# Performance work log

Measured on AMD Instinct MI355X. Metric: run time of the kernel, lower is better.

## Reference

```python
import jax, jax.numpy as jnp
import numpy as np

K = 1024
D = 256
BETA = 0.25


def setup_inputs() -> dict:
    key = jax.random.key(0)
    k1, k2 = jax.random.split(key)
    inputs = jax.random.normal(k1, (16, D, 4096), dtype=jnp.float32)  # (B, D, T)
    # embedding.weight.data.uniform_(-1/K, 1/K)
    weight = jax.random.uniform(k2, (K, D), dtype=jnp.float32, minval=-1.0 / K, maxval=1.0 / K)
    return {"inputs": inputs, "weight": weight}


def reference(inputs, weight):
    B, Dd, T = inputs.shape
    x = jnp.transpose(inputs, (0, 2, 1))          # (B, T, D)
    flat = x.reshape(-1, Dd)                      # (N, D), N = B*T
    in_sqr = jnp.sum(flat * flat, axis=1, keepdims=True)     # (N, 1)
    embed_sqr = jnp.sum(weight * weight, axis=1)             # (K,)
    dis = in_sqr + embed_sqr - 2.0 * (flat @ weight.T)       # (N, K)
    ind = jnp.argmin(dis, axis=1)                            # (N,)
    quant = weight[ind].reshape(B, T, Dd)                    # gather == one-hot @ weight
    vq = jnp.mean((jax.lax.stop_gradient(quant) - x) ** 2)
    commit = jnp.mean((quant - jax.lax.stop_gradient(x)) ** 2)
    vq_loss = BETA * vq + commit
    quant_st = x + jax.lax.stop_gradient(quant - x)          # straight-through
    N = flat.shape[0]
    counts = jnp.zeros((K,), dtype=jnp.float32).at[ind].add(1.0)
    avg_probs = counts / N
    perp = jnp.exp(-jnp.sum(avg_probs * jnp.log(avg_probs + 1e-10)))
    return jnp.transpose(quant_st, (0, 2, 1)), vq_loss, perp
```

## Files before the change

### kernel.cpp

```cpp
#include <hip/hip_runtime.h>
#include <hip/hip_bf16.h>


#define DD   256
#define KK   1024
#define TT   4096
#define BBB  16
#define NROW (BBB*TT)

typedef _Float16 half8 __attribute__((ext_vector_type(8)));
typedef float f32x4 __attribute__((ext_vector_type(4)));

__device__ __forceinline__ unsigned umaxu(unsigned a, unsigned b) { return a > b ? a : b; }
__device__ __forceinline__ unsigned uminu(unsigned a, unsigned b) { return a < b ? a : b; }

__device__ __forceinline__ void gl2lds16(const void* g, void* l) {
    __builtin_amdgcn_global_load_lds(
        (const __attribute__((address_space(1))) unsigned int*)g,
        (__attribute__((address_space(3))) unsigned int*)l,
        16, 0, 0);
}

__global__ void prep(const float* __restrict__ w, _Float16* __restrict__ w16,
                     unsigned* __restrict__ counts, double* __restrict__ lsum,
                     float* __restrict__ wsq) {
    int gid = blockIdx.x * 256 + threadIdx.x;
    int k = gid >> 5;
    int c = gid & 31;
    int chunk = k >> 4, n = k & 15;
    int ks = c >> 2, q = c & 3;
    const float* src = w + (k << 8) + (c << 3);
    union { uint4 u; _Float16 h[8]; } pk;
#pragma unroll
    for (int j = 0; j < 8; ++j) pk.h[j] = (_Float16)(src[j] * 1024.0f);
    size_t dst = ((((size_t)chunk * 8 + ks) * 4 + q) * 16 + n) * 8;
    *(uint4*)(w16 + dst) = pk.u;
    if (c == 0) {
        const float4* wr4 = (const float4*)(w + (k << 8));
        float s = 0.f;
#pragma unroll 8
        for (int ii = 0; ii < 64; ++ii) {
            float4 v = wr4[ii];
            s += v.x * v.x + v.y * v.y + v.z * v.z + v.w * v.w;
        }
        wsq[k] = 512.0f * s;
    }
    if (gid < KK) counts[gid] = 0u;
    if (gid == KK) *lsum = 0.0;
}

__global__ __launch_bounds__(256) void stageA(const float* __restrict__ x,
                                              const _Float16* __restrict__ w16,
                                              const float* __restrict__ wsq,
                                              uint4* __restrict__ cand) {
    __shared__ __align__(16) float wsql[KK];
    __shared__ __align__(16) _Float16 bbuf[2][4096];
    int tid = threadIdx.x, bid = blockIdx.x;
    int b = bid >> 5;
    int t0 = (bid & 31) << 7;
    const float* xbase = x + ((size_t)b << 20) + t0;

    int lane = tid & 63, wv = tid >> 6;
    int n = lane & 15, q = lane >> 4;

    const uint4* wsrc = (const uint4*)w16;

    gl2lds16(wsrc + tid,       (_Float16*)bbuf[0] + (tid << 3));
    gl2lds16(wsrc + tid + 256, (_Float16*)bbuf[0] + ((tid + 256) << 3));

    ((float4*)wsql)[tid] = ((const float4*)wsq)[tid];

    half8 afrag[2][8];
#pragma unroll
    for (int mt = 0; mt < 2; ++mt) {
        int rl = (wv << 5) + (mt << 4) + n;
#pragma unroll
        for (int ks = 0; ks < 8; ++ks) {
            const float* p = xbase + (((size_t)((ks << 5) + (q << 3))) << 12) + rl;
            half8 f;
#pragma unroll
            for (int j = 0; j < 8; ++j) f[j] = (_Float16)p[(size_t)j << 12];
            afrag[mt][ks] = f;
        }
    }
    __syncthreads();

    unsigned b1[8], b2[8];
#pragma unroll
    for (int i = 0; i < 8; ++i) { b1[i] = 0u; b2[i] = 0u; }

    for (int ch = 0; ch < 64; ++ch) {
        if (ch + 1 < 64) {
            const uint4* src = wsrc + ((ch + 1) << 9);
            _Float16* db = bbuf[(ch + 1) & 1];
            gl2lds16(src + tid,       db + (tid << 3));
            gl2lds16(src + tid + 256, db + ((tid + 256) << 3));
        }
        {
            const _Float16* bb = bbuf[ch & 1];
            half8 bfr[8];
#pragma unroll
            for (int ks = 0; ks < 8; ++ks)
                bfr[ks] = *(const half8*)(bb + (ks << 9) + (lane << 3));
            f32x4 a0 = {0.f, 0.f, 0.f, 0.f};
            f32x4 a1 = {0.f, 0.f, 0.f, 0.f};
#pragma unroll
            for (int ks = 0; ks < 8; ++ks) {
                a0 = __builtin_amdgcn_mfma_f32_16x16x32_f16(afrag[0][ks], bfr[ks], a0, 0, 0, 0);
                a1 = __builtin_amdgcn_mfma_f32_16x16x32_f16(afrag[1][ks], bfr[ks], a1, 0, 0, 0);
            }
            unsigned kg = (unsigned)((ch << 4) + n);
            float csub = wsql[kg];
#pragma unroll
            for (int i = 0; i < 4; ++i) {
                float v = fmaxf(a0[i] - csub, 0.0f);
                unsigned p = (__float_as_uint(v) & 0xFFFFFC00u) | kg;
                unsigned o = b1[i];
                b2[i] = umaxu(b2[i], uminu(p, o));
                b1[i] = umaxu(o, p);
                v = fmaxf(a1[i] - csub, 0.0f);
                p = (__float_as_uint(v) & 0xFFFFFC00u) | kg;
                o = b1[4 + i];
                b2[4 + i] = umaxu(b2[4 + i], uminu(p, o));
                b1[4 + i] = umaxu(o, p);
            }
        }
        __syncthreads();
    }

#pragma unroll
    for (int s = 0; s < 8; ++s) {
        unsigned v0 = b1[s], v1 = b2[s], v2 = 0u, v3 = 0u;
#pragma unroll
        for (int m = 1; m <= 8; m <<= 1) {
            unsigned e0 = __shfl_xor(v0, m);
            unsigned e1 = __shfl_xor(v1, m);
            unsigned e2 = __shfl_xor(v2, m);
            unsigned e3 = __shfl_xor(v3, m);
#pragma unroll
            for (int u = 0; u < 4; ++u) {
                unsigned e = (u == 0) ? e0 : (u == 1) ? e1 : (u == 2) ? e2 : e3;
                unsigned t;
                t = umaxu(e, v0); e = uminu(e, v0); v0 = t;
                t = umaxu(e, v1); e = uminu(e, v1); v1 = t;
                t = umaxu(e, v2); e = uminu(e, v2); v2 = t;
                v3 = umaxu(e, v3);
            }
        }
        if (n == 0) {
            int row_local = (wv << 5) + ((s >> 2) << 4) + (q << 2) + (s & 3);
            cand[(bid << 7) + row_local] = make_uint4(v0, v1, v2, v3);
        }
    }
}

#define XLS 257
__global__ __launch_bounds__(256) void stageBC(const float* __restrict__ x,
                                               const float* __restrict__ w,
                                               const uint4* __restrict__ cand,
                                               float* __restrict__ out,
                                               unsigned* __restrict__ counts,
                                               double* __restrict__ lsum) {
    __shared__ __align__(16) float xl[32 * XLS];
    __shared__ double disl[32][4];
    __shared__ int winner[32];
    __shared__ double ldis[32];
    int tid = threadIdx.x, bid = blockIdx.x;
    int b = bid >> 7, t0 = (bid & 127) << 5;
    int lane = tid & 63, wv = tid >> 6;

    {
        int dr = tid >> 3;
        int t4 = (tid & 7) << 2;
        const float* xb = x + ((size_t)b << 20) + t0 + t4;
#pragma unroll
        for (int pass = 0; pass < 8; ++pass) {
            int d = (pass << 5) + dr;
            float4 v = *(const float4*)(xb + ((size_t)d << 12));
            xl[(t4 + 0) * XLS + d] = v.x;
            xl[(t4 + 1) * XLS + d] = v.y;
            xl[(t4 + 2) * XLS + d] = v.z;
            xl[(t4 + 3) * XLS + d] = v.w;
        }
    }
    __syncthreads();

    int c = lane >> 4, dl = lane & 15;
#pragma unroll
    for (int rr = 0; rr < 8; ++rr) {
        int r = (wv << 3) + rr;
        int rowg = (b << 12) + t0 + r;
        unsigned ci = ((const unsigned*)cand)[((size_t)rowg << 2) + c] & 1023u;
        const float* wr = w + (ci << 8);
        double s = 0.0;
#pragma unroll
        for (int dd = 0; dd < 4; ++dd) {
            int d4 = (dd << 6) + (dl << 2);
            float4 xv = *(const float4*)(&xl[r * XLS + d4]);
            float4 wv4 = *(const float4*)(wr + d4);
            double e;
            e = (double)xv.x - (double)wv4.x; s = fma(e, e, s);
            e = (double)xv.y - (double)wv4.y; s = fma(e, e, s);
            e = (double)xv.z - (double)wv4.z; s = fma(e, e, s);
            e = (double)xv.w - (double)wv4.w; s = fma(e, e, s);
        }
#pragma unroll
        for (int m = 1; m <= 8; m <<= 1) s += __shfl_xor(s, m);
        if (dl == 0) disl[r][c] = s;
    }
    __syncthreads();

    if (tid < 32) {
        int rowg = (b << 12) + t0 + tid;
        uint4 cc = cand[rowg];
        unsigned i0 = cc.x & 1023u, i1 = cc.y & 1023u, i2 = cc.z & 1023u, i3 = cc.w & 1023u;
        double dm = disl[tid][0]; unsigned ci = i0;
        double dk;
        dk = disl[tid][1]; if (dk < dm || (dk == dm && i1 < ci)) { dm = dk; ci = i1; }
        dk = disl[tid][2]; if (dk < dm || (dk == dm && i2 < ci)) { dm = dk; ci = i2; }
        dk = disl[tid][3]; if (dk < dm || (dk == dm && i3 < ci)) { dm = dk; ci = i3; }
        winner[tid] = (int)ci;
        ldis[tid] = dm;
        atomicAdd(&counts[ci], 1u);
    }
    __syncthreads();

    float* wg = xl;
#pragma unroll
    for (int rp = 0; rp < 8; ++rp) {
        int r = (rp << 2) + wv;
        int win = winner[r];
        *(float4*)(&wg[r * XLS + (lane << 2)]) =
            *(const float4*)(w + (win << 8) + (lane << 2));
    }
    __syncthreads();

    {
        int dr = tid >> 3;
        int t4 = (tid & 7) << 2;
        float* ob = out + ((size_t)b << 20) + t0 + t4;
#pragma unroll
        for (int pass = 0; pass < 8; ++pass) {
            int d = (pass << 5) + dr;
            float4 o;
            o.x = wg[(t4 + 0) * XLS + d];
            o.y = wg[(t4 + 1) * XLS + d];
            o.z = wg[(t4 + 2) * XLS + d];
            o.w = wg[(t4 + 3) * XLS + d];
            *(float4*)(ob + ((size_t)d << 12)) = o;
        }
    }

    __syncthreads();
    if (tid < 16) ldis[tid] += ldis[tid + 16];
    __syncthreads();
    if (tid < 8) ldis[tid] += ldis[tid + 8];
    __syncthreads();
    if (tid < 4) ldis[tid] += ldis[tid + 4];
    __syncthreads();
    if (tid < 2) ldis[tid] += ldis[tid + 2];
    __syncthreads();
    if (tid == 0) atomicAdd(lsum, ldis[0] + ldis[1]);
}

__global__ void finalize(const unsigned* __restrict__ counts,
                         const double* __restrict__ lsum,
                         float* __restrict__ out2) {
    __shared__ double part[256];
    int tid = threadIdx.x;
    double s = 0.0;
    for (int i = tid; i < KK; i += 256) {
        double p = (double)counts[i] / (double)NROW;
        s += p * log(p + 1e-10);
    }
    part[tid] = s;
    __syncthreads();
    for (int st = 128; st > 0; st >>= 1) {
        if (tid < st) part[tid] += part[tid + st];
        __syncthreads();
    }
    if (tid == 0) {
        out2[0] = (float)(1.25 * (*lsum) / ((double)NROW * (double)DD));
        out2[1] = (float)exp(-part[0]);
    }
}

extern "C" void kernel_launch(void* const* d_in, const int* in_sizes, int n_in,
                              void* d_out, int out_size, void* d_ws, size_t ws_size,
                              hipStream_t stream) {
    const float* x = (const float*)d_in[0];
    const float* w = (const float*)d_in[1];
    float* out = (float*)d_out;
    char* ws = (char*)d_ws;
    _Float16* w16    = (_Float16*)ws;
    uint4*    cnd    = (uint4*)(ws + 524288);
    unsigned* counts = (unsigned*)(ws + 1572864);
    float*    wsq    = (float*)(ws + 1576960);
    double*   lsum   = (double*)(ws + 1581056);

    prep<<<128, 256, 0, stream>>>(w, w16, counts, lsum, wsq);
    stageA<<<512, 256, 0, stream>>>(x, w16, wsq, (uint4*)cnd);
    stageBC<<<2048, 256, 0, stream>>>(x, w, (const uint4*)cnd, out, counts, lsum);
    finalize<<<1, 256, 0, stream>>>(counts, lsum, out + (size_t)NROW * DD);
}
```

Before: 204.8 us.

## Load codebook fragments directly into registers instead of staging through LDS

```diff
diff --git a/kernel.cpp b/kernel.cpp
--- a/kernel.cpp
+++ b/kernel.cpp
@@ -13,13 +13,6 @@
 
 __device__ __forceinline__ unsigned umaxu(unsigned a, unsigned b) { return a > b ? a : b; }
 __device__ __forceinline__ unsigned uminu(unsigned a, unsigned b) { return a < b ? a : b; }
-
-__device__ __forceinline__ void gl2lds16(const void* g, void* l) {
-    __builtin_amdgcn_global_load_lds(
-        (const __attribute__((address_space(1))) unsigned int*)g,
-        (__attribute__((address_space(3))) unsigned int*)l,
-        16, 0, 0);
-}
 
 __global__ void prep(const float* __restrict__ w, _Float16* __restrict__ w16,
                      unsigned* __restrict__ counts, double* __restrict__ lsum,
@@ -54,7 +47,6 @@
                                               const float* __restrict__ wsq,
                                               uint4* __restrict__ cand) {
     __shared__ __align__(16) float wsql[KK];
-    __shared__ __align__(16) _Float16 bbuf[2][4096];
     int tid = threadIdx.x, bid = blockIdx.x;
     int b = bid >> 5;
     int t0 = (bid & 31) << 7;
@@ -63,11 +55,6 @@
     int lane = tid & 63, wv = tid >> 6;
     int n = lane & 15, q = lane >> 4;
 
-    const uint4* wsrc = (const uint4*)w16;
-
-    gl2lds16(wsrc + tid,       (_Float16*)bbuf[0] + (tid << 3));
-    gl2lds16(wsrc + tid + 256, (_Float16*)bbuf[0] + ((tid + 256) << 3));
-
     ((float4*)wsql)[tid] = ((const float4*)wsq)[tid];
 
     half8 afrag[2][8];
@@ -89,43 +76,53 @@
 #pragma unroll
     for (int i = 0; i < 8; ++i) { b1[i] = 0u; b2[i] = 0u; }
 
-    for (int ch = 0; ch < 64; ++ch) {
-        if (ch + 1 < 64) {
-            const uint4* src = wsrc + ((ch + 1) << 9);
-            _Float16* db = bbuf[(ch + 1) & 1];
-            gl2lds16(src + tid,       db + (tid << 3));
-            gl2lds16(src + tid + 256, db + ((tid + 256) << 3));
-        }
+    const uint4* wsrc = (const uint4*)w16;
+
+    half8 bufA[8], bufB[8];
+#pragma unroll
+    for (int ks = 0; ks < 8; ++ks)
+        bufA[ks] = *(const half8*)(wsrc + (ks << 6) + lane);
+
+    auto compute = [&](int ch, const half8* bfr) {
+        f32x4 a0 = {0.f, 0.f, 0.f, 0.f};
+        f32x4 a1 = {0.f, 0.f, 0.f, 0.f};
+#pragma unroll
+        for (int ks = 0; ks < 8; ++ks) {
+            a0 = __builtin_amdgcn_mfma_f32_16x16x32_f16(afrag[0][ks], bfr[ks], a0, 0, 0, 0);
+            a1 = __builtin_amdgcn_mfma_f32_16x16x32_f16(afrag[1][ks], bfr[ks], a1, 0, 0, 0);
+        }
+        unsigned kg = (unsigned)((ch << 4) + n);
+        float csub = wsql[kg];
+#pragma unroll
+        for (int i = 0; i < 4; ++i) {
+            float v = fmaxf(a0[i] - csub, 0.0f);
+            unsigned p = (__float_as_uint(v) & 0xFFFFFC00u) | kg;
+            unsigned o = b1[i];
+            b2[i] = umaxu(b2[i], uminu(p, o));
+            b1[i] = umaxu(o, p);
+            v = fmaxf(a1[i] - csub, 0.0f);
+            p = (__float_as_uint(v) & 0xFFFFFC00u) | kg;
+            o = b1[4 + i];
+            b2[4 + i] = umaxu(b2[4 + i], uminu(p, o));
+            b1[4 + i] = umaxu(o, p);
+        }
+    };
+
+    for (int ch = 0; ch < 64; ch += 2) {
         {
-            const _Float16* bb = bbuf[ch & 1];
-            half8 bfr[8];
+            const uint4* p = wsrc + (((ch + 1) & 63) << 9) + lane;
 #pragma unroll
             for (int ks = 0; ks < 8; ++ks)
-                bfr[ks] = *(const half8*)(bb + (ks << 9) + (lane << 3));
-            f32x4 a0 = {0.f, 0.f, 0.f, 0.f};
-            f32x4 a1 = {0.f, 0.f, 0.f, 0.f};
-#pragma unroll
-            for (int ks = 0; ks < 8; ++ks) {
-                a0 = __builtin_amdgcn_mfma_f32_16x16x32_f16(afrag[0][ks], bfr[ks], a0, 0, 0, 0);
-                a1 = __builtin_amdgcn_mfma_f32_16x16x32_f16(afrag[1][ks], bfr[ks], a1, 0, 0, 0);
-            }
-            unsigned kg = (unsigned)((ch << 4) + n);
-            float csub = wsql[kg];
-#pragma unroll
-            for (int i = 0; i < 4; ++i) {
-                float v = fmaxf(a0[i] - csub, 0.0f);
-                unsigned p = (__float_as_uint(v) & 0xFFFFFC00u) | kg;
-                unsigned o = b1[i];
-                b2[i] = umaxu(b2[i], uminu(p, o));
-                b1[i] = umaxu(o, p);
-                v = fmaxf(a1[i] - csub, 0.0f);
-                p = (__float_as_uint(v) & 0xFFFFFC00u) | kg;
-                o = b1[4 + i];
-                b2[4 + i] = umaxu(b2[4 + i], uminu(p, o));
-                b1[4 + i] = umaxu(o, p);
-            }
-        }
-        __syncthreads();
+                bufB[ks] = *(const half8*)(p + (ks << 6));
+        }
+        compute(ch, bufA);
+        {
+            const uint4* p = wsrc + (((ch + 2) & 63) << 9) + lane;
+#pragma unroll
+            for (int ks = 0; ks < 8; ++ks)
+                bufA[ks] = *(const half8*)(p + (ks << 6));
+        }
+        compute(ch + 1, bufB);
     }
 
 #pragma unroll
```

Result: faster. 197.7 us (-3.5%).

## Pre-transpose inputs to fp16 MFMA layout and triple-buffer codebook loads

Applied to the files above, without the earlier changes.

```diff
diff --git a/kernel.cpp b/kernel.cpp
--- a/kernel.cpp
+++ b/kernel.cpp
@@ -49,55 +49,99 @@
     if (gid == KK) *lsum = 0.0;
 }
 
-__global__ __launch_bounds__(256) void stageA(const float* __restrict__ x,
-                                              const _Float16* __restrict__ w16,
-                                              const float* __restrict__ wsq,
-                                              uint4* __restrict__ cand) {
+#define XPS 260
+__global__ __launch_bounds__(256) void xprep(const float* __restrict__ x,
+                                             _Float16* __restrict__ xf16) {
+    __shared__ __align__(16) float xt[32 * XPS];
+    int tid = threadIdx.x, bid = blockIdx.x;
+    int b = bid >> 7, t0 = (bid & 127) << 5;
+    const float* xb = x + ((size_t)b << 20) + t0;
+
+    {
+        int dr = tid >> 3;
+        int t4 = (tid & 7) << 2;
+#pragma unroll
+        for (int pass = 0; pass < 8; ++pass) {
+            int d = (pass << 5) + dr;
+            float4 v = *(const float4*)(xb + ((size_t)d << 12) + t4);
+            xt[(t4 + 0) * XPS + d] = v.x;
+            xt[(t4 + 1) * XPS + d] = v.y;
+            xt[(t4 + 2) * XPS + d] = v.z;
+            xt[(t4 + 3) * XPS + d] = v.w;
+        }
+    }
+    __syncthreads();
+
+    int tgg0 = (b << 8) + (t0 >> 4);
+#pragma unroll
+    for (int f = 0; f < 4; ++f) {
+        int idx = (f << 8) + tid;
+        int tg = idx >> 9;
+        int ks = (idx >> 6) & 7;
+        int ln = idx & 63;
+        int n2 = ln & 15, q2 = ln >> 4;
+        int tl = (tg << 4) + n2;
+        int db = (ks << 5) + (q2 << 3);
+        float4 u0 = *(const float4*)(&xt[tl * XPS + db]);
+        float4 u1 = *(const float4*)(&xt[tl * XPS + db + 4]);
+        union { uint4 u; _Float16 h[8]; } pk;
+        pk.h[0] = (_Float16)u0.x; pk.h[1] = (_Float16)u0.y;
+        pk.h[2] = (_Float16)u0.z; pk.h[3] = (_Float16)u0.w;
+        pk.h[4] = (_Float16)u1.x; pk.h[5] = (_Float16)u1.y;
+        pk.h[6] = (_Float16)u1.z; pk.h[7] = (_Float16)u1.w;
+        size_t dst = ((((size_t)(tgg0 + tg) << 3) + ks) * 64 + ln) << 3;
+        *(uint4*)(xf16 + dst) = pk.u;
+    }
+}
+
+
+#define STAGE(chn) do {                                                        \
+    const uint4* _s = wsrc + (((chn) & 63) << 9) + tid;                        \
+    _Float16* _d = bbuf[(chn) % 3];                                            \
+    gl2lds16(_s,       _d + (tid << 3));                                       \
+    gl2lds16(_s + 256, _d + ((tid + 256) << 3));                               \
+} while (0)
+
+__global__ __launch_bounds__(256, 2) void stageA(const _Float16* __restrict__ xf16,
+                                                 const _Float16* __restrict__ w16,
+                                                 const float* __restrict__ wsq,
+                                                 uint4* __restrict__ cand) {
     __shared__ __align__(16) float wsql[KK];
-    __shared__ __align__(16) _Float16 bbuf[2][4096];
+    __shared__ __align__(16) _Float16 bbuf[3][4096];
     int tid = threadIdx.x, bid = blockIdx.x;
     int b = bid >> 5;
     int t0 = (bid & 31) << 7;
-    const float* xbase = x + ((size_t)b << 20) + t0;
 
     int lane = tid & 63, wv = tid >> 6;
     int n = lane & 15, q = lane >> 4;
 
     const uint4* wsrc = (const uint4*)w16;
 
-    gl2lds16(wsrc + tid,       (_Float16*)bbuf[0] + (tid << 3));
-    gl2lds16(wsrc + tid + 256, (_Float16*)bbuf[0] + ((tid + 256) << 3));
-
+    half8 afrag[2][8];
+#pragma unroll
+    for (int mt = 0; mt < 2; ++mt) {
+        int tgg = (b << 8) + (t0 >> 4) + (wv << 1) + mt;
+#pragma unroll
+        for (int ks = 0; ks < 8; ++ks) {
+            const _Float16* ap = xf16 + (((((size_t)tgg << 3) + ks) * 64 + lane) << 3);
+            afrag[mt][ks] = *(const half8*)ap;
+        }
+    }
     ((float4*)wsql)[tid] = ((const float4*)wsq)[tid];
 
-    half8 afrag[2][8];
-#pragma unroll
-    for (int mt = 0; mt < 2; ++mt) {
-        int rl = (wv << 5) + (mt << 4) + n;
-#pragma unroll
-        for (int ks = 0; ks < 8; ++ks) {
-            const float* p = xbase + (((size_t)((ks << 5) + (q << 3))) << 12) + rl;
-            half8 f;
-#pragma unroll
-            for (int j = 0; j < 8; ++j) f[j] = (_Float16)p[(size_t)j << 12];
-            afrag[mt][ks] = f;
-        }
-    }
-    __syncthreads();
+    STAGE(0);
+    STAGE(1);
 
     unsigned b1[8], b2[8];
 #pragma unroll
     for (int i = 0; i < 8; ++i) { b1[i] = 0u; b2[i] = 0u; }
 
     for (int ch = 0; ch < 64; ++ch) {
-        if (ch + 1 < 64) {
-            const uint4* src = wsrc + ((ch + 1) << 9);
-            _Float16* db = bbuf[(ch + 1) & 1];
-            gl2lds16(src + tid,       db + (tid << 3));
-            gl2lds16(src + tid + 256, db + ((tid + 256) << 3));
-        }
+        STAGE(ch + 2);
+        asm volatile("s_waitcnt vmcnt(4) lgkmcnt(0)" ::: "memory");
+        __builtin_amdgcn_s_barrier();
         {
-            const _Float16* bb = bbuf[ch & 1];
+            const _Float16* bb = bbuf[ch % 3];
             half8 bfr[8];
 #pragma unroll
             for (int ks = 0; ks < 8; ++ks)
@@ -113,9 +157,10 @@
             float csub = wsql[kg];
 #pragma unroll
             for (int i = 0; i < 4; ++i) {
-                float v = fmaxf(a0[i] - csub, 0.0f);
-                unsigned p = (__float_as_uint(v) & 0xFFFFFC00u) | kg;
-                unsigned o = b1[i];
+                float v; unsigned p, o;
+                v = fmaxf(a0[i] - csub, 0.0f);
+                p = (__float_as_uint(v) & 0xFFFFFC00u) | kg;
+                o = b1[i];
                 b2[i] = umaxu(b2[i], uminu(p, o));
                 b1[i] = umaxu(o, p);
                 v = fmaxf(a1[i] - csub, 0.0f);
@@ -125,7 +170,8 @@
                 b1[4 + i] = umaxu(o, p);
             }
         }
-        __syncthreads();
+        asm volatile("s_waitcnt lgkmcnt(0)" ::: "memory");
+        __builtin_amdgcn_s_barrier();
     }
 
 #pragma unroll
@@ -297,9 +343,11 @@
     unsigned* counts = (unsigned*)(ws + 1572864);
     float*    wsq    = (float*)(ws + 1576960);
     double*   lsum   = (double*)(ws + 1581056);
+    _Float16* xf16   = (_Float16*)d_out;
 
     prep<<<128, 256, 0, stream>>>(w, w16, counts, lsum, wsq);
-    stageA<<<512, 256, 0, stream>>>(x, w16, wsq, (uint4*)cnd);
+    xprep<<<2048, 256, 0, stream>>>(x, xf16);
+    stageA<<<512, 256, 0, stream>>>(xf16, w16, wsq, (uint4*)cnd);
     stageBC<<<2048, 256, 0, stream>>>(x, w, (const uint4*)cnd, out, counts, lsum);
     finalize<<<1, 256, 0, stream>>>(counts, lsum, out + (size_t)NROW * DD);
 }
```

Result: slower. 215.7 us (+5.3%).
